# Optimization experiments

Hardware: AMD Instinct MI355X
Metric: run time of the kernel (lower is better)

The kernel has to match this reference:

```python
import jax, jax.numpy as jnp
import numpy as np

NUM_HEADS = 16


def setup_inputs() -> dict:
    key = jax.random.key(0)
    k1, k2, k3, k4 = jax.random.split(key, 4)
    B, N, C = 4, 1024, 1024
    x = jax.random.normal(k1, (B, N, C), dtype=jnp.float32)
    mask = jnp.ones((B, N), dtype=jnp.float32)  # 1 = visible token
    # 0.02 init scale keeps logits in a sane range (avoids saturated softmax)
    W_qkv = jax.random.normal(k2, (C, 3 * C), dtype=jnp.float32) * 0.02
    W_proj = jax.random.normal(k3, (C, C), dtype=jnp.float32) * 0.02
    b_proj = jax.random.normal(k4, (C,), dtype=jnp.float32) * 0.02
    return {"x": x, "mask": mask, "W_qkv": W_qkv, "W_proj": W_proj, "b_proj": b_proj}


def reference(x, mask, W_qkv, W_proj, b_proj):
    B, N, C = x.shape
    H = NUM_HEADS
    D = C // H
    scale = D ** -0.5
    qkv = (x @ W_qkv).reshape(B, N, 3, H, D)
    q, k, v = qkv[:, :, 0], qkv[:, :, 1], qkv[:, :, 2]  # each [B, N, H, D]
    attn = jnp.einsum("bnhd,bmhd->bhnm", q, k) * scale  # [B, H, N, N]
    attn = attn + (1.0 - mask)[:, None, None, :] * -5.0  # additive mask penalty
    attn = jax.nn.softmax(attn, axis=-1)
    out = jnp.einsum("bhnm,bmhd->bnhd", attn, v).reshape(B, N, C)
    return out @ W_proj + b_proj
```

## Files before the change

### kernel.cpp

```cpp
#include <hip/hip_runtime.h>

typedef __attribute__((ext_vector_type(8))) short bf16x8;
typedef __attribute__((ext_vector_type(4))) float f32x4;
typedef __attribute__((ext_vector_type(16))) float f32x16;
typedef __attribute__((ext_vector_type(4))) float fl4;
typedef __attribute__((ext_vector_type(8))) unsigned short u16x8;
typedef __attribute__((ext_vector_type(4))) unsigned short u16x4;
typedef __attribute__((ext_vector_type(2))) int i32x2;
typedef __attribute__((ext_vector_type(4))) int i32x4;

#define MFMA16(A,B,C) __builtin_amdgcn_mfma_f32_16x16x32_bf16((A),(B),(C),0,0,0)
#define MFMA32(A,B,C) __builtin_amdgcn_mfma_f32_32x32x16_bf16((A),(B),(C),0,0,0)

#if __has_builtin(__builtin_amdgcn_exp2f)
#define EXP2R(x) __builtin_amdgcn_exp2f(x)
#else
#define EXP2R(x) exp2f(x)
#endif

__device__ __forceinline__ unsigned short f2bf_bits(float x) {
  union { float f; unsigned u; } v; v.f = x;
  unsigned r = v.u + 0x7fffu + ((v.u >> 16) & 1u);
  return (unsigned short)(r >> 16);
}

__device__ __forceinline__ void gload_lds16(const void* g, void* l) {
  __builtin_amdgcn_global_load_lds((const __attribute__((address_space(1))) void*)g,
                                   (__attribute__((address_space(3))) void*)l, 16, 0, 0);
}

__device__ __forceinline__ int cvtpk_bf16(float a, float b) {
  int r; asm("v_cvt_pk_bf16_f32 %0, %1, %2" : "=v"(r) : "v"(a), "v"(b)); return r;
}

__device__ __forceinline__ void plswap(int& a, int& b) {
#if __has_builtin(__builtin_amdgcn_permlane32_swap)
  i32x2 r = __builtin_amdgcn_permlane32_swap(a, b, false, false);
  a = r[0]; b = r[1];
#else
  asm volatile("s_nop 1\n\tv_permlane32_swap_b32 %0, %1" : "+v"(a), "+v"(b));
#endif
}

__global__ __launch_bounds__(256) void k_prep(const float* __restrict__ x,
                                              unsigned short* __restrict__ xb,
                                              const float* __restrict__ wqkv,
                                              unsigned short* __restrict__ dqkv,
                                              const float* __restrict__ wproj,
                                              unsigned short* __restrict__ dproj) {
  __shared__ float tile[64][65];
  const int bid = blockIdx.x;
  const int t = threadIdx.x;
  if (bid < 2048) {
    int i = (bid * 256 + t) * 8;
    fl4 a = *(const fl4*)(x + i);
    fl4 b = *(const fl4*)(x + i + 4);
    u16x8 o;
    o[0] = f2bf_bits(a[0]); o[1] = f2bf_bits(a[1]); o[2] = f2bf_bits(a[2]); o[3] = f2bf_bits(a[3]);
    o[4] = f2bf_bits(b[0]); o[5] = f2bf_bits(b[1]); o[6] = f2bf_bits(b[2]); o[7] = f2bf_bits(b[3]);
    *(u16x8*)(xb + i) = o;
    return;
  }
  const int idx = bid - 2048;
  const int bx = idx & 63, by = idx >> 6;
  const float* src; unsigned short* dst; int NCOL, nt;
  if (bx < 48) { src = wqkv; dst = dqkv; NCOL = 3072; nt = bx * 64; }
  else         { src = wproj; dst = dproj; NCOL = 1024; nt = (bx - 48) * 64; }
  const float sc = (bx < 16) ? 0.18033688f : 1.0f;
  const int kt = by * 64;
  {
    int r = t >> 2, c0 = (t & 3) * 16;
    const float* s = src + (size_t)(kt + r) * NCOL + nt + c0;
    #pragma unroll
    for (int j = 0; j < 4; ++j) {
      fl4 v = *(const fl4*)(s + j * 4);
      tile[r][c0 + j * 4 + 0] = v[0]; tile[r][c0 + j * 4 + 1] = v[1];
      tile[r][c0 + j * 4 + 2] = v[2]; tile[r][c0 + j * 4 + 3] = v[3];
    }
  }
  __syncthreads();
  {
    int n = t >> 2, kc = (t & 3) * 16;
    unsigned short* d = dst + (size_t)(nt + n) * 1024 + kt + kc;
    u16x8 o0, o1;
    #pragma unroll
    for (int j = 0; j < 8; ++j) o0[j] = f2bf_bits(tile[kc + j][n] * sc);
    #pragma unroll
    for (int j = 0; j < 8; ++j) o1[j] = f2bf_bits(tile[kc + 8 + j][n] * sc);
    *(u16x8*)d = o0;
    *(u16x8*)(d + 8) = o1;
  }
}

template <int MODE>
__global__ __launch_bounds__(256) void k_gemm(const unsigned short* __restrict__ A,
                                              const unsigned short* __restrict__ Bt,
                                              unsigned short* __restrict__ qp,
                                              unsigned short* __restrict__ kp,
                                              unsigned short* __restrict__ vtp,
                                              const float* __restrict__ bias,
                                              float* __restrict__ outp) {
  __shared__ __align__(16) char lds[49152];
  const int tid = threadIdx.x, lane = tid & 63, w = tid >> 6;
  const int wm = w >> 1, wn = w & 1;
  const int bid = blockIdx.x;
  const int xcd = bid & 7, s = bid >> 3;
  int ry, cx;
  if (MODE == 0) { ry = (xcd & 3) * 8 + s / 12; cx = (xcd >> 2) * 12 + s % 12; }
  else           { ry = xcd * 4 + s / 8;        cx = s % 8; }
  const int m0 = ry * 128, n0 = cx * 128;
  const char* Ab = (const char*)A + (size_t)m0 * 2048;
  const char* Bb = (const char*)Bt + (size_t)n0 * 2048;

  int goff[2];
  #pragma unroll
  for (int i = 0; i < 2; ++i) {
    int c = i * 256 + tid;
    int lr = c >> 3, sl = c & 7, p = sl >> 2, kc = (sl & 3) ^ (lr & 3);
    goff[i] = (((lr << 1) | p) * 2048) + (kc << 4);
  }

  int afo[4], bfo[4];
  #pragma unroll
  for (int mi = 0; mi < 4; ++mi) {
    int tr = wm * 64 + mi * 16 + (lane & 15), kc = lane >> 4;
    afo[mi] = (tr >> 1) * 128 + (tr & 1) * 64 + (((kc ^ ((tr >> 1) & 3))) << 4);
  }
  #pragma unroll
  for (int ni = 0; ni < 4; ++ni) {
    int tr = wn * 64 + ni * 16 + (lane & 15), kc = lane >> 4;
    bfo[ni] = (tr >> 1) * 128 + (tr & 1) * 64 + (((kc ^ ((tr >> 1) & 3))) << 4);
  }

  f32x4 acc[4][4];
  #pragma unroll
  for (int mi = 0; mi < 4; ++mi)
    #pragma unroll
    for (int ni = 0; ni < 4; ++ni) acc[mi][ni] = f32x4{0.f, 0.f, 0.f, 0.f};

#define GSTAGE(BUF, T)                                                         \
  do {                                                                         \
    char* dA = lds + (BUF) * 16384 + tid * 16;                                 \
    char* dB = dA + 8192;                                                      \
    gload_lds16(Ab + goff[0] + (T) * 64, dA);                                  \
    gload_lds16(Ab + goff[1] + (T) * 64, dA + 4096);                           \
    gload_lds16(Bb + goff[0] + (T) * 64, dB);                                  \
    gload_lds16(Bb + goff[1] + (T) * 64, dB + 4096);                           \
  } while (0)

#define GCOMP(BUF)                                                             \
  do {                                                                         \
    const char* LA = lds + (BUF) * 16384;                                      \
    const char* LB = LA + 8192;                                                \
    bf16x8 af[4], bfv[4];                                                      \
    _Pragma("unroll") for (int mi = 0; mi < 4; ++mi)                           \
      af[mi] = *(const bf16x8*)(LA + afo[mi]);                                 \
    _Pragma("unroll") for (int ni = 0; ni < 4; ++ni)                           \
      bfv[ni] = *(const bf16x8*)(LB + bfo[ni]);                                \
    _Pragma("unroll") for (int mi = 0; mi < 4; ++mi)                           \
      _Pragma("unroll") for (int ni = 0; ni < 4; ++ni)                         \
        acc[mi][ni] = MFMA16(af[mi], bfv[ni], acc[mi][ni]);                    \
  } while (0)

  GSTAGE(0, 0);
  GSTAGE(1, 1);
  {
    int bc = 0, bs = 2;
    for (int j = 0; j < 31; ++j) {
      asm volatile("s_waitcnt vmcnt(4)" ::: "memory");
      __builtin_amdgcn_s_barrier();
      if (j < 30) GSTAGE(bs, j + 2);
      GCOMP(bc);
      bc = (bc == 2) ? 0 : bc + 1;
      bs = (bs == 2) ? 0 : bs + 1;
    }
    asm volatile("s_waitcnt vmcnt(0)" ::: "memory");
    __builtin_amdgcn_s_barrier();
    GCOMP(1);
  }
#undef GCOMP
#undef GSTAGE

  if (MODE == 0) {
    #pragma unroll
    for (int mi = 0; mi < 4; ++mi) {
      int row0 = m0 + wm * 64 + mi * 16 + ((lane >> 4) << 2);
      int bb = row0 >> 10, nn0 = row0 & 1023;
      #pragma unroll
      for (int ni = 0; ni < 4; ++ni) {
        int col = n0 + wn * 64 + ni * 16 + (lane & 15);
        int tt = col >> 10, rem = col & 1023, h = rem >> 6, d = rem & 63;
        f32x4 a = acc[mi][ni];
        if (tt == 2) {
          u16x4 pv;
          pv[0] = f2bf_bits(a[0]); pv[1] = f2bf_bits(a[1]);
          pv[2] = f2bf_bits(a[2]); pv[3] = f2bf_bits(a[3]);
          *(u16x4*)(vtp + (((size_t)(bb * 16 + h) * 64 + d) << 10) + nn0) = pv;
        } else {
          unsigned short* dst = (tt == 0) ? qp : kp;
          size_t base = ((size_t)(bb * 16 + h)) << 16;
          #pragma unroll
          for (int r = 0; r < 4; ++r)
            dst[base + (size_t)(nn0 + r) * 64 + d] = f2bf_bits(a[r]);
        }
      }
    }
  } else {
    #pragma unroll
    for (int mi = 0; mi < 4; ++mi) {
      int row0 = m0 + wm * 64 + mi * 16 + ((lane >> 4) << 2);
      #pragma unroll
      for (int ni = 0; ni < 4; ++ni) {
        int col = n0 + wn * 64 + ni * 16 + (lane & 15);
        float bv = bias[col];
        f32x4 a = acc[mi][ni];
        #pragma unroll
        for (int r = 0; r < 4; ++r)
          outp[(size_t)(row0 + r) * 1024 + col] = a[r] + bv;
      }
    }
  }
}

__global__ __launch_bounds__(512, 4) void k_attn(const unsigned short* __restrict__ qp,
                                                 const unsigned short* __restrict__ kp,
                                                 const unsigned short* __restrict__ vtp,
                                                 const float* __restrict__ mask,
                                                 unsigned short* __restrict__ aop) {
  __shared__ __align__(16) char lds[49152];
  const int tid = threadIdx.x, lane = tid & 63, w = tid >> 6;
  const int hi = lane >> 5, lq = lane & 31;
  const int pair = w >> 2, qsub = w & 3;
  const int g = blockIdx.x;
  const int bh = (g & 7) * 8 + ((g >> 6) & 7);
  const int qc = (g >> 3) & 7;
  const int b = bh >> 4, h = bh & 15;
  const char* kb = (const char*)(kp + ((size_t)bh << 16));
  const char* vb = (const char*)(vtp + ((size_t)bh << 16));
  const unsigned short* qh = qp + ((size_t)bh << 16);
  const float* mrow = mask + b * 1024 + pair * 512;
  const int q0 = qc * 128 + qsub * 32;

  const int kpk = tid >> 8, krow = (tid >> 3) & 31, kslot = tid & 7;
  const char* gK = kb + (size_t)kpk * 65536 + (size_t)krow * 128
                   + ((kslot ^ (krow & 7)) * 16);
  const int vpk = tid >> 8, vrow = (tid >> 2) & 63, vslot = tid & 3;
  const char* gV = vb + (size_t)vpk * 1024 + (size_t)vrow * 2048
                   + ((vslot ^ ((vrow >> 1) & 3)) * 16);
  char* const dK = lds + tid * 16;
  char* const dV = lds + 8192 + tid * 16;

  int kfo[4], vfo[4];
  #pragma unroll
  for (int dc = 0; dc < 4; ++dc)
    kfo[dc] = lq * 128 + (((dc << 1) | hi) ^ (lq & 7)) * 16;
  #pragma unroll
  for (int ks = 0; ks < 2; ++ks)
    #pragma unroll
    for (int nb = 0; nb < 2; ++nb) {
      int row = nb * 32 + lq;
      vfo[ks * 2 + nb] = row * 64 + (((ks << 1) | hi) ^ ((row >> 1) & 3)) * 16;
    }

  int bws[16];
  #pragma unroll
  for (int t2 = 0; t2 < 16; ++t2) {
    float mv = mrow[t2 * 32 + lq];
    bws[t2] = (hi == 0) ? (int)f2bf_bits(fmaf(mv, 7.2134752f, -12.9842554f)) : 0;
  }

  bf16x8 qB[4];
  #pragma unroll
  for (int dc = 0; dc < 4; ++dc)
    qB[dc] = *(const bf16x8*)(qh + (q0 + lq) * 64 + dc * 16 + hi * 8);

  i32x4 onesw = {hi == 0 ? 0x3F80 : 0, 0, 0, 0};
  const bf16x8 onesB = __builtin_bit_cast(bf16x8, onesw);

  f32x16 Z16;
  #pragma unroll
  for (int i = 0; i < 16; ++i) Z16[i] = 0.f;

  f32x16 O0, O1;
  #pragma unroll
  for (int i = 0; i < 16; ++i) { O0[i] = 0.f; O1[i] = 0.f; }
  float lsum = 0.f;

#define STAGE(BUF, T)                                                          \
  do {                                                                         \
    gload_lds16(gK + (T) * 4096, dK + (BUF) * 16384);                          \
    gload_lds16(gV + (T) * 64,   dV + (BUF) * 16384);                          \
  } while (0)

#define VMCNT(N) asm volatile("s_waitcnt vmcnt(" #N ")" ::: "memory")

#define STEP(BUF, T, N)                                                        \
  do {                                                                         \
    VMCNT(N);                                                                  \
    __builtin_amdgcn_s_barrier();                                              \
    if ((T) + 2 <= 15) STAGE(((T) + 2) % 3, (T) + 2);                          \
    const char* K = lds + (BUF) * 16384 + pair * 4096;                         \
    const char* V = lds + (BUF) * 16384 + 8192 + pair * 4096;                  \
    f32x16 acc;                                                                \
    {                                                                          \
      i32x4 bwv = {bws[T], 0, 0, 0};                                           \
      acc = MFMA32(__builtin_bit_cast(bf16x8, bwv), onesB, Z16);               \
    }                                                                          \
    __builtin_amdgcn_s_setprio(1);                                             \
    _Pragma("unroll") for (int dc = 0; dc < 4; ++dc) {                         \
      bf16x8 kf = *(const bf16x8*)(K + kfo[dc]);                               \
      acc = MFMA32(kf, qB[dc], acc);                                           \
    }                                                                          \
    __builtin_amdgcn_s_setprio(0);                                             \
    float p[16];                                                               \
    _Pragma("unroll") for (int r = 0; r < 16; ++r) {                           \
      p[r] = EXP2R(acc[r]);                                                    \
      lsum += p[r];                                                            \
    }                                                                          \
    int X0 = cvtpk_bf16(p[0], p[1]),   X1 = cvtpk_bf16(p[2], p[3]);            \
    int Y0 = cvtpk_bf16(p[4], p[5]),   Y1 = cvtpk_bf16(p[6], p[7]);            \
    int Z0 = cvtpk_bf16(p[8], p[9]),   Z1 = cvtpk_bf16(p[10], p[11]);          \
    int W0 = cvtpk_bf16(p[12], p[13]), W1 = cvtpk_bf16(p[14], p[15]);          \
    plswap(X0, Y0); plswap(X1, Y1);                                            \
    plswap(Z0, W0); plswap(Z1, W1);                                            \
    i32x4 pa0v = {X0, X1, Y0, Y1};                                             \
    i32x4 pa1v = {Z0, Z1, W0, W1};                                             \
    const bf16x8 PA0 = __builtin_bit_cast(bf16x8, pa0v);                       \
    const bf16x8 PA1 = __builtin_bit_cast(bf16x8, pa1v);                       \
    bf16x8 va0 = *(const bf16x8*)(V + vfo[0]);                                 \
    bf16x8 va1 = *(const bf16x8*)(V + vfo[1]);                                 \
    bf16x8 vb0 = *(const bf16x8*)(V + vfo[2]);                                 \
    bf16x8 vb1 = *(const bf16x8*)(V + vfo[3]);                                 \
    __builtin_amdgcn_s_setprio(1);                                             \
    O0 = MFMA32(PA0, va0, O0);                                                 \
    O1 = MFMA32(PA0, va1, O1);                                                 \
    O0 = MFMA32(PA1, vb0, O0);                                                 \
    O1 = MFMA32(PA1, vb1, O1);                                                 \
    __builtin_amdgcn_s_setprio(0);                                             \
  } while (0)

  STAGE(0, 0);
  STAGE(1, 1);
  STEP(0, 0, 2);  STEP(1, 1, 2);  STEP(2, 2, 2);  STEP(0, 3, 2);
  STEP(1, 4, 2);  STEP(2, 5, 2);  STEP(0, 6, 2);  STEP(1, 7, 2);
  STEP(2, 8, 2);  STEP(0, 9, 2);  STEP(1, 10, 2); STEP(2, 11, 2);
  STEP(0, 12, 2); STEP(1, 13, 2); STEP(2, 14, 2); STEP(0, 15, 0);
#undef STEP
#undef VMCNT
#undef STAGE

  __syncthreads();
  float tot = lsum + __shfl_xor(lsum, 32);
  float* fx = (float*)lds;
  if (pair == 1) {
    int base = qsub * 64 * 34 + lane * 34;
    #pragma unroll
    for (int r = 0; r < 16; ++r) { fx[base + r] = O0[r]; fx[base + 16 + r] = O1[r]; }
    fx[base + 32] = tot;
  }
  __syncthreads();
  if (pair == 0) {
    int base = qsub * 64 * 34 + lane * 34;
    float invT = 1.0f / (tot + fx[base + 32]);
    #pragma unroll
    for (int r = 0; r < 16; ++r) {
      int qr = (r & 3) + 8 * (r >> 2) + 4 * hi;
      float iv = __shfl(invT, qr);
      float o0 = (O0[r] + fx[base + r]) * iv;
      float o1 = (O1[r] + fx[base + 16 + r]) * iv;
      size_t ob = (size_t)(b * 1024 + q0 + qr) * 1024 + h * 64 + lq;
      aop[ob] = f2bf_bits(o0);
      aop[ob + 32] = f2bf_bits(o1);
    }
  }
}

extern "C" void kernel_launch(void* const* d_in, const int* in_sizes, int n_in,
                              void* d_out, int out_size, void* d_ws, size_t ws_size,
                              hipStream_t stream) {
  const float* x     = (const float*)d_in[0];
  const float* mask  = (const float*)d_in[1];
  const float* wqkv  = (const float*)d_in[2];
  const float* wproj = (const float*)d_in[3];
  const float* bproj = (const float*)d_in[4];
  float* out = (float*)d_out;

  char* ws = (char*)d_ws;
  unsigned short* xb     = (unsigned short*)(ws);
  unsigned short* wqkvt  = (unsigned short*)(ws + 8388608);
  unsigned short* wprojt = (unsigned short*)(ws + 14680064);
  unsigned short* qbuf   = (unsigned short*)(ws + 16777216);
  unsigned short* kbuf   = (unsigned short*)(ws + 25165824);
  unsigned short* vtbuf  = (unsigned short*)(ws + 33554432);
  unsigned short* aobuf  = (unsigned short*)(ws + 41943040);

  k_prep<<<dim3(3072), dim3(256), 0, stream>>>(x, xb, wqkv, wqkvt, wproj, wprojt);
  k_gemm<0><<<dim3(768), dim3(256), 0, stream>>>(xb, wqkvt, qbuf, kbuf, vtbuf, nullptr, nullptr);
  k_attn<<<dim3(512), dim3(512), 0, stream>>>(qbuf, kbuf, vtbuf, mask, aobuf);
  k_gemm<1><<<dim3(256), dim3(256), 0, stream>>>(aobuf, wprojt, nullptr, nullptr, nullptr, bproj, out);
}
```

Before: 89.49 us.

## Switch attention K/V staging to double-buffered 64-key tiles with 8 steps

The attention kernel drops its triple-buffered 32-key pipeline, which had 16 barrier steps. It now uses a double-buffered pipeline that stages 64 keys per step and processes two 32-key windows between barriers, halving the number of barriers and waits. LDS per block grows from 48 KB to 64 KB, and the V swizzle layout is changed to match the K layout. Each step now waits for vmcnt(0), so prefetch depth is one tile instead of two, which may expose more load latency and lower occupancy.

```diff
diff --git a/kernel.cpp b/kernel.cpp
--- a/kernel.cpp
+++ b/kernel.cpp
@@ -227,7 +227,7 @@
                                                  const unsigned short* __restrict__ vtp,
                                                  const float* __restrict__ mask,
                                                  unsigned short* __restrict__ aop) {
-  __shared__ __align__(16) char lds[49152];
+  __shared__ __align__(16) char lds[65536];
   const int tid = threadIdx.x, lane = tid & 63, w = tid >> 6;
   const int hi = lane >> 5, lq = lane & 31;
   const int pair = w >> 2, qsub = w & 3;
@@ -241,26 +241,20 @@
   const float* mrow = mask + b * 1024 + pair * 512;
   const int q0 = qc * 128 + qsub * 32;
 
-  const int kpk = tid >> 8, krow = (tid >> 3) & 31, kslot = tid & 7;
-  const char* gK = kb + (size_t)kpk * 65536 + (size_t)krow * 128
-                   + ((kslot ^ (krow & 7)) * 16);
-  const int vpk = tid >> 8, vrow = (tid >> 2) & 63, vslot = tid & 3;
-  const char* gV = vb + (size_t)vpk * 1024 + (size_t)vrow * 2048
-                   + ((vslot ^ ((vrow >> 1) & 3)) * 16);
-  char* const dK = lds + tid * 16;
-  char* const dV = lds + 8192 + tid * 16;
+  const int srow = tid >> 3, sslot = tid & 7;
+  const int scc = sslot ^ (srow & 7);
+  const char* gK = kb + (size_t)srow * 128 + scc * 16;
+  const char* gV = vb + (size_t)srow * 2048 + scc * 16;
 
   int kfo[4], vfo[4];
   #pragma unroll
   for (int dc = 0; dc < 4; ++dc)
-    kfo[dc] = lq * 128 + (((dc << 1) | hi) ^ (lq & 7)) * 16;
+    kfo[dc] = lq * 128 + ((((dc << 1) | hi) ^ (lq & 7)) << 4);
   #pragma unroll
   for (int ks = 0; ks < 2; ++ks)
     #pragma unroll
-    for (int nb = 0; nb < 2; ++nb) {
-      int row = nb * 32 + lq;
-      vfo[ks * 2 + nb] = row * 64 + (((ks << 1) | hi) ^ ((row >> 1) & 3)) * 16;
-    }
+    for (int nb = 0; nb < 2; ++nb)
+      vfo[ks * 2 + nb] = (nb * 32 + lq) * 128 + ((((ks << 1) | hi) ^ (lq & 7)) << 4);
 
   int bws[16];
   #pragma unroll
@@ -288,27 +282,23 @@
 
 #define STAGE(BUF, T)                                                          \
   do {                                                                         \
-    gload_lds16(gK + (T) * 4096, dK + (BUF) * 16384);                          \
-    gload_lds16(gV + (T) * 64,   dV + (BUF) * 16384);                          \
-  } while (0)
-
-#define VMCNT(N) asm volatile("s_waitcnt vmcnt(" #N ")" ::: "memory")
-
-#define STEP(BUF, T, N)                                                        \
-  do {                                                                         \
-    VMCNT(N);                                                                  \
-    __builtin_amdgcn_s_barrier();                                              \
-    if ((T) + 2 <= 15) STAGE(((T) + 2) % 3, (T) + 2);                          \
-    const char* K = lds + (BUF) * 16384 + pair * 4096;                         \
-    const char* V = lds + (BUF) * 16384 + 8192 + pair * 4096;                  \
+    char* d0 = lds + (BUF) * 32768 + tid * 16;                                 \
+    gload_lds16(gK + (T) * 8192,         d0);                                  \
+    gload_lds16(gK + (T) * 8192 + 65536, d0 + 8192);                           \
+    gload_lds16(gV + (T) * 128,          d0 + 16384);                          \
+    gload_lds16(gV + (T) * 128 + 1024,   d0 + 24576);                          \
+  } while (0)
+
+#define WINDOW(KP, VP, BW, VX)                                                 \
+  do {                                                                         \
     f32x16 acc;                                                                \
     {                                                                          \
-      i32x4 bwv = {bws[T], 0, 0, 0};                                           \
+      i32x4 bwv = {(BW), 0, 0, 0};                                             \
       acc = MFMA32(__builtin_bit_cast(bf16x8, bwv), onesB, Z16);               \
     }                                                                          \
     __builtin_amdgcn_s_setprio(1);                                             \
     _Pragma("unroll") for (int dc = 0; dc < 4; ++dc) {                         \
-      bf16x8 kf = *(const bf16x8*)(K + kfo[dc]);                               \
+      bf16x8 kf = *(const bf16x8*)((KP) + kfo[dc]);                            \
       acc = MFMA32(kf, qB[dc], acc);                                           \
     }                                                                          \
     __builtin_amdgcn_s_setprio(0);                                             \
@@ -327,10 +317,10 @@
     i32x4 pa1v = {Z0, Z1, W0, W1};                                             \
     const bf16x8 PA0 = __builtin_bit_cast(bf16x8, pa0v);                       \
     const bf16x8 PA1 = __builtin_bit_cast(bf16x8, pa1v);                       \
-    bf16x8 va0 = *(const bf16x8*)(V + vfo[0]);                                 \
-    bf16x8 va1 = *(const bf16x8*)(V + vfo[1]);                                 \
-    bf16x8 vb0 = *(const bf16x8*)(V + vfo[2]);                                 \
-    bf16x8 vb1 = *(const bf16x8*)(V + vfo[3]);                                 \
+    bf16x8 va0 = *(const bf16x8*)((VP) + (vfo[0] ^ (VX)));                     \
+    bf16x8 va1 = *(const bf16x8*)((VP) + (vfo[1] ^ (VX)));                     \
+    bf16x8 vb0 = *(const bf16x8*)((VP) + (vfo[2] ^ (VX)));                     \
+    bf16x8 vb1 = *(const bf16x8*)((VP) + (vfo[3] ^ (VX)));                     \
     __builtin_amdgcn_s_setprio(1);                                             \
     O0 = MFMA32(PA0, va0, O0);                                                 \
     O1 = MFMA32(PA0, va1, O1);                                                 \
@@ -339,14 +329,22 @@
     __builtin_amdgcn_s_setprio(0);                                             \
   } while (0)
 
+#define STEP(BUF, T, LAST)                                                     \
+  do {                                                                         \
+    asm volatile("s_waitcnt vmcnt(0)" ::: "memory");                           \
+    __builtin_amdgcn_s_barrier();                                              \
+    if (!(LAST)) STAGE((BUF) ^ 1, (T) + 1);                                    \
+    const char* K = lds + (BUF) * 32768 + pair * 8192;                         \
+    const char* V = lds + (BUF) * 32768 + 16384 + pair * 8192;                 \
+    WINDOW(K, V, bws[2 * (T)], 0);                                             \
+    WINDOW(K + 4096, V, bws[2 * (T) + 1], 64);                                 \
+  } while (0)
+
   STAGE(0, 0);
-  STAGE(1, 1);
-  STEP(0, 0, 2);  STEP(1, 1, 2);  STEP(2, 2, 2);  STEP(0, 3, 2);
-  STEP(1, 4, 2);  STEP(2, 5, 2);  STEP(0, 6, 2);  STEP(1, 7, 2);
-  STEP(2, 8, 2);  STEP(0, 9, 2);  STEP(1, 10, 2); STEP(2, 11, 2);
-  STEP(0, 12, 2); STEP(1, 13, 2); STEP(2, 14, 2); STEP(0, 15, 0);
+  STEP(0, 0, 0); STEP(1, 1, 0); STEP(0, 2, 0); STEP(1, 3, 0);
+  STEP(0, 4, 0); STEP(1, 5, 0); STEP(0, 6, 0); STEP(1, 7, 1);
 #undef STEP
-#undef VMCNT
+#undef WINDOW
 #undef STAGE
 
   __syncthreads();
```

Result: no change. 90.73 us (+1.4%).
